# Kernel tuning notes

Measured on AMD Instinct MI355X. Metric: run time of the kernel, lower is better.

Reference implementation:

```python
import jax, jax.numpy as jnp
import numpy as np

B, D, H = 32768, 256, 8
DH = D // H
SCALE = 1.0 / float(np.sqrt(DH))
# neighbor indices: for query node i, context = the other 3 nodes (in order)
NEIGH = np.array([[1, 2, 3], [0, 2, 3], [0, 1, 3], [0, 1, 2]], dtype=np.int32)


def setup_inputs() -> dict:
    key = jax.random.key(0)
    ks = jax.random.split(key, 6)
    s = 0.02
    mk = lambda k: jax.random.normal(k, (D, D), jnp.float32) * s
    return {
        "tokens": jax.random.normal(ks[0], (B, 4, D), jnp.float32),
        "Wq": mk(ks[1]),
        "Wk": mk(ks[2]),
        "Wv": mk(ks[3]),
        "Wr": mk(ks[4]),
        "Wo": mk(ks[5]),
        "ln_g": jnp.ones((D,), jnp.float32),
        "ln_b": jnp.zeros((D,), jnp.float32),
    }


def reference(tokens, Wq, Wk, Wv, Wr, Wo, ln_g, ln_b):
    # tokens: [B,4,D]. All 4 modality queries share one GCA block (share_gca=True),
    # so we batch the 4-node complete-graph message passing into one pass.
    neigh = jnp.asarray(NEIGH)
    ctx = tokens[:, neigh]                    # [B,4,3,D]
    Q = tokens @ Wq.T                         # [B,4,D]
    K = ctx @ Wk.T                            # [B,4,3,D]
    V = ctx @ Wv.T
    R = ctx @ Wr.T
    V_eff = jax.nn.sigmoid(R) * V             # gated values
    Qh = Q.reshape(B, 4, H, DH)
    Kh = K.reshape(B, 4, 3, H, DH)
    Vh = V_eff.reshape(B, 4, 3, H, DH)
    scores = jnp.einsum('bihd,bilhd->bihl', Qh, Kh) * SCALE   # [B,4,H,3]
    attn = jax.nn.softmax(scores, axis=-1)    # dropout = identity (eval mode)
    out = jnp.einsum('bihl,bilhd->bihd', attn, Vh).reshape(B, 4, D)
    out = out @ Wo.T
    y = tokens + out                          # residual
    mu = y.mean(-1, keepdims=True)
    var = y.var(-1, keepdims=True)
    y = (y - mu) / jnp.sqrt(var + 1e-5) * ln_g + ln_b   # LayerNorm
    # attn: [B,4,H,3] -> per-query attn maps (attn[:, i] == attn for modality-i query, [B,H,1,3] squeezed)
    return y, attn
```

## Files before the change

### kernel.cpp

```cpp
#include <hip/hip_runtime.h>
#include <stdint.h>


#define D_DIM   256
#define H_NUM   8
#define RT      64
#define NTHR    512
#define ROWS_TOT 131072
#define Y_SZ    33554432
#define SCALE_F 0.17677669529663687f
#define W_ELEMS 65536
#define WS_NEED (5 * W_ELEMS * 2)

#define SX_LD   264
#define AO_LD   264
#define SP_LD   20

typedef __attribute__((ext_vector_type(8))) short bf16x8;
typedef __attribute__((ext_vector_type(4))) float f32x4;

__device__ __forceinline__ float b2f(uint16_t s) {
    union { uint32_t u; float f; } c; c.u = ((uint32_t)s) << 16; return c.f;
}
__device__ __forceinline__ uint16_t f2b(float f) {
    union { float f; uint32_t u; } c; c.f = f;
    return (uint16_t)((c.u + 0x7fffu + ((c.u >> 16) & 1u)) >> 16);
}
__device__ __forceinline__ bf16x8 cvt8(const float* p) {
    const float4 a = *(const float4*)p;
    const float4 b = *(const float4*)(p + 4);
    bf16x8 r;
    r[0] = (short)f2b(a.x); r[1] = (short)f2b(a.y);
    r[2] = (short)f2b(a.z); r[3] = (short)f2b(a.w);
    r[4] = (short)f2b(b.x); r[5] = (short)f2b(b.y);
    r[6] = (short)f2b(b.z); r[7] = (short)f2b(b.w);
    return r;
}
__device__ __forceinline__ uint2 pack4(f32x4 a) {
    uint2 p;
    p.x = (uint32_t)f2b(a[0]) | ((uint32_t)f2b(a[1]) << 16);
    p.y = (uint32_t)f2b(a[2]) | ((uint32_t)f2b(a[3]) << 16);
    return p;
}

__global__ __launch_bounds__(256)
void conv_weights(const float* __restrict__ Wq, const float* __restrict__ Wk,
                  const float* __restrict__ Wv, const float* __restrict__ Wr,
                  const float* __restrict__ Wo, uint16_t* __restrict__ dst)
{
    const int m = blockIdx.x >> 6;
    const float* src = (m == 0) ? Wq : (m == 1) ? Wk : (m == 2) ? Wv
                     : (m == 3) ? Wr : Wo;
    const int base = (blockIdx.x & 63) * 1024 + threadIdx.x * 4;
    const float4 v = *(const float4*)&src[base];
    uint2 pk;
    pk.x = (uint32_t)f2b(v.x) | ((uint32_t)f2b(v.y) << 16);
    pk.y = (uint32_t)f2b(v.z) | ((uint32_t)f2b(v.w) << 16);
    *(uint2*)&dst[(size_t)m * W_ELEMS + base] = pk;
}

template<bool WBF16>
__global__ __launch_bounds__(NTHR, 2)
void cmaa_fused(const float* __restrict__ tok,
                const float* __restrict__ Wq, const float* __restrict__ Wk,
                const float* __restrict__ Wv, const float* __restrict__ Wr,
                const float* __restrict__ Wo,
                const uint16_t* __restrict__ wbf,
                const float* __restrict__ lng, const float* __restrict__ lnb,
                float* __restrict__ outp)
{
    __shared__ __align__(16) uint16_t sX  [RT * SX_LD];
    __shared__ __align__(16) uint16_t sAO [RT * AO_LD];
    __shared__ __align__(16) float    sALf[RT * H_NUM * 3];
    __shared__ __align__(16) float    sPT [RT * SP_LD];

    const int tid  = threadIdx.x;
    const int wv   = tid >> 6;
    const int lane = tid & 63;
    const int l15  = lane & 15;
    const int quad = lane >> 4;
    const int R0   = blockIdx.x * RT;

    {
        const float* g = tok + (size_t)R0 * D_DIM;
        #pragma unroll
        for (int it = 0; it < 4; ++it) {
            const int t = tid + it * NTHR;
            const int row = t >> 5, c = t & 31;
            *(bf16x8*)&sX[row * SX_LD + c * 8] = cvt8(&g[row * D_DIM + c * 8]);
        }
    }
    __syncthreads();

    const bool qk = (wv < 4);
    const int  hl = wv & 3;

    bf16x8 wo_reg[2][8];

    #pragma unroll
    for (int p = 0; p < 2; ++p) {
        const int h = p * 4 + hl;
        const int colbase = h * 32;
        const float*    WF0 = qk ? Wq : Wv;
        const float*    WF1 = qk ? Wk : Wr;
        const uint16_t* WB0 = wbf + (size_t)(qk ? 0 : 2) * W_ELEMS;
        const uint16_t* WB1 = WB0 + W_ELEMS;

        bf16x8 w0[2][8], w1[2][8];
        #pragma unroll
        for (int ct = 0; ct < 2; ++ct) {
            const int wrow = colbase + ct * 16 + l15;
            #pragma unroll
            for (int kk = 0; kk < 8; ++kk) {
                if constexpr (WBF16) {
                    w0[ct][kk] = *(const bf16x8*)&WB0[(size_t)wrow * D_DIM + kk * 32 + quad * 8];
                    w1[ct][kk] = *(const bf16x8*)&WB1[(size_t)wrow * D_DIM + kk * 32 + quad * 8];
                } else {
                    w0[ct][kk] = cvt8(&WF0[(size_t)wrow * D_DIM + kk * 32 + quad * 8]);
                    w1[ct][kk] = cvt8(&WF1[(size_t)wrow * D_DIM + kk * 32 + quad * 8]);
                }
            }
        }

        f32x4 acc[2][2][4];
        #pragma unroll
        for (int m = 0; m < 2; ++m)
            #pragma unroll
            for (int ct = 0; ct < 2; ++ct)
                #pragma unroll
                for (int nt = 0; nt < 4; ++nt)
                    acc[m][ct][nt] = (f32x4){0.f, 0.f, 0.f, 0.f};

        #pragma unroll
        for (int kk = 0; kk < 8; ++kk) {
            const int k0 = kk * 32;
            bf16x8 ax[4];
            #pragma unroll
            for (int nt = 0; nt < 4; ++nt)
                ax[nt] = *(const bf16x8*)&sX[(nt * 16 + l15) * SX_LD + k0 + quad * 8];
            #pragma unroll
            for (int ct = 0; ct < 2; ++ct)
                #pragma unroll
                for (int nt = 0; nt < 4; ++nt)
                    acc[0][ct][nt] = __builtin_amdgcn_mfma_f32_16x16x32_bf16(w0[ct][kk], ax[nt], acc[0][ct][nt], 0, 0, 0);
            #pragma unroll
            for (int ct = 0; ct < 2; ++ct)
                #pragma unroll
                for (int nt = 0; nt < 4; ++nt)
                    acc[1][ct][nt] = __builtin_amdgcn_mfma_f32_16x16x32_bf16(w1[ct][kk], ax[nt], acc[1][ct][nt], 0, 0, 0);
        }

        if (p == 1) {
            const uint16_t* WoB = wbf + (size_t)4 * W_ELEMS;
            #pragma unroll
            for (int ct = 0; ct < 2; ++ct) {
                const int wrow = wv * 32 + ct * 16 + l15;
                #pragma unroll
                for (int kk = 0; kk < 8; ++kk) {
                    if constexpr (WBF16)
                        wo_reg[ct][kk] = *(const bf16x8*)&WoB[(size_t)wrow * D_DIM + kk * 32 + quad * 8];
                    else
                        wo_reg[ct][kk] = cvt8(&Wo[(size_t)wrow * D_DIM + kk * 32 + quad * 8]);
                }
            }
        }

        if (qk) {
            #pragma unroll
            for (int nt = 0; nt < 4; ++nt) {
                float sc[3];
                #pragma unroll
                for (int m = 1; m <= 3; ++m) {
                    float s = 0.f;
                    #pragma unroll
                    for (int ct = 0; ct < 2; ++ct)
                        #pragma unroll
                        for (int r = 0; r < 4; ++r)
                            s += acc[0][ct][nt][r] * __shfl_xor(acc[1][ct][nt][r], m);
                    s += __shfl_xor(s, 16);
                    s += __shfl_xor(s, 32);
                    sc[m - 1] = s * SCALE_F;
                }
                const float mx = fmaxf(sc[0], fmaxf(sc[1], sc[2]));
                const float e1 = __expf(sc[0] - mx), e2 = __expf(sc[1] - mx), e3 = __expf(sc[2] - mx);
                const float inv = 1.f / (e1 + e2 + e3);
                const float am[3] = { e1 * inv, e2 * inv, e3 * inv };
                const int token = nt * 16 + l15;
                if (quad == 0) {
                    const int ii = token & 3;
                    float* al = &sALf[(token * H_NUM + h) * 3];
                    #pragma unroll
                    for (int l = 0; l < 3; ++l) {
                        const int jj = l + (l >= ii);
                        const int m  = ii ^ jj;
                        al[l] = am[m - 1];
                    }
                }
            }
        } else {
            #pragma unroll
            for (int ct = 0; ct < 2; ++ct)
                #pragma unroll
                for (int nt = 0; nt < 4; ++nt)
                    #pragma unroll
                    for (int r = 0; r < 4; ++r)
                        acc[0][ct][nt][r] *= 1.f / (1.f + __expf(-acc[1][ct][nt][r]));
        }
        __syncthreads();

        if (!qk) {
            #pragma unroll
            for (int nt = 0; nt < 4; ++nt) {
                const int token = nt * 16 + l15;
                const int ii = token & 3;
                const float* al = &sALf[(token * H_NUM + h) * 3];
                float am[3];
                #pragma unroll
                for (int m = 1; m <= 3; ++m) {
                    const int jj = ii ^ m;
                    const int l  = jj - (jj > ii ? 1 : 0);
                    am[m - 1] = al[l];
                }
                #pragma unroll
                for (int ct = 0; ct < 2; ++ct) {
                    f32x4 ao;
                    #pragma unroll
                    for (int r = 0; r < 4; ++r) {
                        const float v = acc[0][ct][nt][r];
                        ao[r] = am[0] * __shfl_xor(v, 1)
                              + am[1] * __shfl_xor(v, 2)
                              + am[2] * __shfl_xor(v, 3);
                    }
                    *(uint2*)&sAO[token * AO_LD + colbase + ct * 16 + quad * 4] = pack4(ao);
                }
            }
        }
        __syncthreads();
    }

    if (tid < 384) {
        const float4 v = *(const float4*)&sALf[tid * 4];
        *(float4*)&outp[Y_SZ + (size_t)R0 * (H_NUM * 3) + tid * 4] = v;
    }

    f32x4 acc3[2][4];
    #pragma unroll
    for (int ct = 0; ct < 2; ++ct)
        #pragma unroll
        for (int nt = 0; nt < 4; ++nt)
            acc3[ct][nt] = (f32x4){0.f, 0.f, 0.f, 0.f};

    #pragma unroll
    for (int kk = 0; kk < 8; ++kk) {
        const int k0 = kk * 32;
        bf16x8 ao[4];
        #pragma unroll
        for (int nt = 0; nt < 4; ++nt)
            ao[nt] = *(const bf16x8*)&sAO[(nt * 16 + l15) * AO_LD + k0 + quad * 8];
        #pragma unroll
        for (int ct = 0; ct < 2; ++ct)
            #pragma unroll
            for (int nt = 0; nt < 4; ++nt)
                acc3[ct][nt] = __builtin_amdgcn_mfma_f32_16x16x32_bf16(wo_reg[ct][kk], ao[nt], acc3[ct][nt], 0, 0, 0);
    }

    #pragma unroll
    for (int nt = 0; nt < 4; ++nt) {
        const int token = nt * 16 + l15;
        float s1 = 0.f, s2 = 0.f;
        #pragma unroll
        for (int ct = 0; ct < 2; ++ct) {
            const ushort4 xv = *(const ushort4*)&sX[token * SX_LD + wv * 32 + ct * 16 + quad * 4];
            const float x0 = b2f(xv.x), x1 = b2f(xv.y), x2 = b2f(xv.z), x3 = b2f(xv.w);
            acc3[ct][nt][0] += x0; acc3[ct][nt][1] += x1;
            acc3[ct][nt][2] += x2; acc3[ct][nt][3] += x3;
            #pragma unroll
            for (int r = 0; r < 4; ++r) {
                const float y = acc3[ct][nt][r];
                s1 += y; s2 += y * y;
            }
        }
        s1 += __shfl_xor(s1, 16); s1 += __shfl_xor(s1, 32);
        s2 += __shfl_xor(s2, 16); s2 += __shfl_xor(s2, 32);
        if (quad == 0) {
            float2 ps; ps.x = s1; ps.y = s2;
            *(float2*)&sPT[token * SP_LD + wv * 2] = ps;
        }
    }
    __syncthreads();

    #pragma unroll
    for (int nt = 0; nt < 4; ++nt) {
        const int token = nt * 16 + l15;
        const f32x4* pp = (const f32x4*)&sPT[token * SP_LD];
        const f32x4 q0 = pp[0], q1 = pp[1], q2 = pp[2], q3 = pp[3];
        const float s1 = q0[0] + q0[2] + q1[0] + q1[2] + q2[0] + q2[2] + q3[0] + q3[2];
        const float s2 = q0[1] + q0[3] + q1[1] + q1[3] + q2[1] + q2[3] + q3[1] + q3[3];
        const float mean = s1 * (1.f / 256.f);
        const float var  = fmaxf(s2 * (1.f / 256.f) - mean * mean, 0.f);
        const float rstd = rsqrtf(var + 1e-5f);
        float* orow = outp + (size_t)(R0 + token) * D_DIM;
        #pragma unroll
        for (int ct = 0; ct < 2; ++ct) {
            const int c0 = wv * 32 + ct * 16 + quad * 4;
            const float4 g4 = *(const float4*)&lng[c0];
            const float4 b4 = *(const float4*)&lnb[c0];
            float4 o4;
            o4.x = (acc3[ct][nt][0] - mean) * rstd * g4.x + b4.x;
            o4.y = (acc3[ct][nt][1] - mean) * rstd * g4.y + b4.y;
            o4.z = (acc3[ct][nt][2] - mean) * rstd * g4.z + b4.z;
            o4.w = (acc3[ct][nt][3] - mean) * rstd * g4.w + b4.w;
            *(float4*)&orow[c0] = o4;
        }
    }
}

extern "C" void kernel_launch(void* const* d_in, const int* in_sizes, int n_in,
                              void* d_out, int out_size, void* d_ws, size_t ws_size,
                              hipStream_t stream) {
    (void)in_sizes; (void)n_in; (void)out_size;
    const float* tok = (const float*)d_in[0];
    const float* Wq  = (const float*)d_in[1];
    const float* Wk  = (const float*)d_in[2];
    const float* Wv  = (const float*)d_in[3];
    const float* Wr  = (const float*)d_in[4];
    const float* Wo  = (const float*)d_in[5];
    const float* lng = (const float*)d_in[6];
    const float* lnb = (const float*)d_in[7];
    float* outp = (float*)d_out;
    uint16_t* wbf = (uint16_t*)d_ws;

    dim3 grid(ROWS_TOT / RT), block(NTHR);
    if (ws_size >= (size_t)WS_NEED) {
        conv_weights<<<dim3(320), dim3(256), 0, stream>>>(Wq, Wk, Wv, Wr, Wo, wbf);
        cmaa_fused<true><<<grid, block, 0, stream>>>(
            tok, Wq, Wk, Wv, Wr, Wo, wbf, lng, lnb, outp);
    } else {
        cmaa_fused<false><<<grid, block, 0, stream>>>(
            tok, Wq, Wk, Wv, Wr, Wo, wbf, lng, lnb, outp);
    }
}
```

Measured before the change: 452.1 us.

## Process two 64-row tiles per block to reuse register-held weights

Each block now handles 128 rows as two 64-row tiles. The Q/K/V/R weight fragments loaded into registers for each head pair are reused across both tiles, and Wo is loaded once after the projection loop. Grid size is halved and the shared-memory buffers are doubled. The intent is to halve global weight reloads per row, at the cost of about double LDS use (likely one block per CU instead of two) and higher register pressure from the two-tile output accumulator.

Result: faster. 414.9 us (-8.2%).

```diff
diff --git a/kernel.cpp b/kernel.cpp
--- a/kernel.cpp
+++ b/kernel.cpp
@@ -69,25 +69,28 @@
                 const float* __restrict__ lng, const float* __restrict__ lnb,
                 float* __restrict__ outp)
 {
-    __shared__ __align__(16) uint16_t sX  [RT * SX_LD];
-    __shared__ __align__(16) uint16_t sAO [RT * AO_LD];
-    __shared__ __align__(16) float    sALf[RT * H_NUM * 3];
-    __shared__ __align__(16) float    sPT [RT * SP_LD];
+    __shared__ __align__(16) uint16_t sX  [2][RT * SX_LD];
+    __shared__ __align__(16) uint16_t sAO [2][RT * AO_LD];
+    __shared__ __align__(16) float    sALf[2][RT * H_NUM * 3];
+    __shared__ __align__(16) float    sPT [2][RT * SP_LD];
 
     const int tid  = threadIdx.x;
     const int wv   = tid >> 6;
     const int lane = tid & 63;
     const int l15  = lane & 15;
     const int quad = lane >> 4;
-    const int R0   = blockIdx.x * RT;
+    const int R0   = blockIdx.x * (2 * RT);
 
     {
         const float* g = tok + (size_t)R0 * D_DIM;
         #pragma unroll
-        for (int it = 0; it < 4; ++it) {
-            const int t = tid + it * NTHR;
-            const int row = t >> 5, c = t & 31;
-            *(bf16x8*)&sX[row * SX_LD + c * 8] = cvt8(&g[row * D_DIM + c * 8]);
+        for (int it = 0; it < 8; ++it) {
+            const int t   = tid + it * NTHR;
+            const int row = t >> 5;
+            const int c   = t & 31;
+            const int tl  = row >> 6;
+            const int rin = row & 63;
+            *(bf16x8*)&sX[tl][rin * SX_LD + c * 8] = cvt8(&g[row * D_DIM + c * 8]);
         }
     }
     __syncthreads();
@@ -95,9 +98,6 @@
     const bool qk = (wv < 4);
     const int  hl = wv & 3;
 
-    bf16x8 wo_reg[2][8];
-
-    #pragma unroll
     for (int p = 0; p < 2; ++p) {
         const int h = p * 4 + hl;
         const int colbase = h * 32;
@@ -123,49 +123,36 @@
         }
 
         f32x4 acc[2][2][4];
-        #pragma unroll
-        for (int m = 0; m < 2; ++m)
-            #pragma unroll
-            for (int ct = 0; ct < 2; ++ct)
+
+        auto gemm = [&](int t) {
+            #pragma unroll
+            for (int m = 0; m < 2; ++m)
+                #pragma unroll
+                for (int ct = 0; ct < 2; ++ct)
+                    #pragma unroll
+                    for (int nt = 0; nt < 4; ++nt)
+                        acc[m][ct][nt] = (f32x4){0.f, 0.f, 0.f, 0.f};
+            #pragma unroll
+            for (int kk = 0; kk < 8; ++kk) {
+                const int k0 = kk * 32;
+                bf16x8 ax[4];
                 #pragma unroll
                 for (int nt = 0; nt < 4; ++nt)
-                    acc[m][ct][nt] = (f32x4){0.f, 0.f, 0.f, 0.f};
-
-        #pragma unroll
-        for (int kk = 0; kk < 8; ++kk) {
-            const int k0 = kk * 32;
-            bf16x8 ax[4];
-            #pragma unroll
-            for (int nt = 0; nt < 4; ++nt)
-                ax[nt] = *(const bf16x8*)&sX[(nt * 16 + l15) * SX_LD + k0 + quad * 8];
-            #pragma unroll
-            for (int ct = 0; ct < 2; ++ct)
-                #pragma unroll
-                for (int nt = 0; nt < 4; ++nt)
-                    acc[0][ct][nt] = __builtin_amdgcn_mfma_f32_16x16x32_bf16(w0[ct][kk], ax[nt], acc[0][ct][nt], 0, 0, 0);
-            #pragma unroll
-            for (int ct = 0; ct < 2; ++ct)
-                #pragma unroll
-                for (int nt = 0; nt < 4; ++nt)
-                    acc[1][ct][nt] = __builtin_amdgcn_mfma_f32_16x16x32_bf16(w1[ct][kk], ax[nt], acc[1][ct][nt], 0, 0, 0);
-        }
-
-        if (p == 1) {
-            const uint16_t* WoB = wbf + (size_t)4 * W_ELEMS;
-            #pragma unroll
-            for (int ct = 0; ct < 2; ++ct) {
-                const int wrow = wv * 32 + ct * 16 + l15;
-                #pragma unroll
-                for (int kk = 0; kk < 8; ++kk) {
-                    if constexpr (WBF16)
-                        wo_reg[ct][kk] = *(const bf16x8*)&WoB[(size_t)wrow * D_DIM + kk * 32 + quad * 8];
-                    else
-                        wo_reg[ct][kk] = cvt8(&Wo[(size_t)wrow * D_DIM + kk * 32 + quad * 8]);
-                }
-            }
-        }
-
-        if (qk) {
+                    ax[nt] = *(const bf16x8*)&sX[t][(nt * 16 + l15) * SX_LD + k0 + quad * 8];
+                #pragma unroll
+                for (int ct = 0; ct < 2; ++ct)
+                    #pragma unroll
+                    for (int nt = 0; nt < 4; ++nt)
+                        acc[0][ct][nt] = __builtin_amdgcn_mfma_f32_16x16x32_bf16(w0[ct][kk], ax[nt], acc[0][ct][nt], 0, 0, 0);
+                #pragma unroll
+                for (int ct = 0; ct < 2; ++ct)
+                    #pragma unroll
+                    for (int nt = 0; nt < 4; ++nt)
+                        acc[1][ct][nt] = __builtin_amdgcn_mfma_f32_16x16x32_bf16(w1[ct][kk], ax[nt], acc[1][ct][nt], 0, 0, 0);
+            }
+        };
+
+        auto qk_post = [&](int t) {
             #pragma unroll
             for (int nt = 0; nt < 4; ++nt) {
                 float sc[3];
@@ -188,7 +175,7 @@
                 const int token = nt * 16 + l15;
                 if (quad == 0) {
                     const int ii = token & 3;
-                    float* al = &sALf[(token * H_NUM + h) * 3];
+                    float* al = &sALf[t][(token * H_NUM + h) * 3];
                     #pragma unroll
                     for (int l = 0; l < 3; ++l) {
                         const int jj = l + (l >= ii);
@@ -197,7 +184,9 @@
                     }
                 }
             }
-        } else {
+        };
+
+        auto v_post = [&]() {
             #pragma unroll
             for (int ct = 0; ct < 2; ++ct)
                 #pragma unroll
@@ -205,15 +194,14 @@
                     #pragma unroll
                     for (int r = 0; r < 4; ++r)
                         acc[0][ct][nt][r] *= 1.f / (1.f + __expf(-acc[1][ct][nt][r]));
-        }
-        __syncthreads();
-
-        if (!qk) {
+        };
+
+        auto pv = [&](int t) {
             #pragma unroll
             for (int nt = 0; nt < 4; ++nt) {
                 const int token = nt * 16 + l15;
                 const int ii = token & 3;
-                const float* al = &sALf[(token * H_NUM + h) * 3];
+                const float* al = &sALf[t][(token * H_NUM + h) * 3];
                 float am[3];
                 #pragma unroll
                 for (int m = 1; m <= 3; ++m) {
@@ -231,86 +219,121 @@
                               + am[1] * __shfl_xor(v, 2)
                               + am[2] * __shfl_xor(v, 3);
                     }
-                    *(uint2*)&sAO[token * AO_LD + colbase + ct * 16 + quad * 4] = pack4(ao);
-                }
-            }
-        }
+                    *(uint2*)&sAO[t][token * AO_LD + colbase + ct * 16 + quad * 4] = pack4(ao);
+                }
+            }
+        };
+
+        gemm(0);
+        if (qk) qk_post(0); else v_post();
         __syncthreads();
-    }
-
-    if (tid < 384) {
-        const float4 v = *(const float4*)&sALf[tid * 4];
-        *(float4*)&outp[Y_SZ + (size_t)R0 * (H_NUM * 3) + tid * 4] = v;
-    }
-
-    f32x4 acc3[2][4];
+        if (!qk) pv(0);
+        gemm(1);
+        if (qk) qk_post(1); else v_post();
+        __syncthreads();
+        if (!qk) pv(1);
+    }
+
+    bf16x8 wo_reg[2][8];
+    {
+        const uint16_t* WoB = wbf + (size_t)4 * W_ELEMS;
+        #pragma unroll
+        for (int ct = 0; ct < 2; ++ct) {
+            const int wrow = wv * 32 + ct * 16 + l15;
+            #pragma unroll
+            for (int kk = 0; kk < 8; ++kk) {
+                if constexpr (WBF16)
+                    wo_reg[ct][kk] = *(const bf16x8*)&WoB[(size_t)wrow * D_DIM + kk * 32 + quad * 8];
+                else
+                    wo_reg[ct][kk] = cvt8(&Wo[(size_t)wrow * D_DIM + kk * 32 + quad * 8]);
+            }
+        }
+    }
+    __syncthreads();
+
+    {
+        const float* sa = &sALf[0][0];
+        #pragma unroll
+        for (int i = tid; i < 768; i += NTHR) {
+            const float4 v = *(const float4*)&sa[i * 4];
+            *(float4*)&outp[Y_SZ + (size_t)R0 * 24 + (size_t)i * 4] = v;
+        }
+    }
+
+    f32x4 acc3[2][2][4];
     #pragma unroll
-    for (int ct = 0; ct < 2; ++ct)
-        #pragma unroll
-        for (int nt = 0; nt < 4; ++nt)
-            acc3[ct][nt] = (f32x4){0.f, 0.f, 0.f, 0.f};
+    for (int t = 0; t < 2; ++t) {
+        #pragma unroll
+        for (int ct = 0; ct < 2; ++ct)
+            #pragma unroll
+            for (int nt = 0; nt < 4; ++nt)
+                acc3[t][ct][nt] = (f32x4){0.f, 0.f, 0.f, 0.f};
+
+        #pragma unroll
+        for (int kk = 0; kk < 8; ++kk) {
+            const int k0 = kk * 32;
+            bf16x8 ao[4];
+            #pragma unroll
+            for (int nt = 0; nt < 4; ++nt)
+                ao[nt] = *(const bf16x8*)&sAO[t][(nt * 16 + l15) * AO_LD + k0 + quad * 8];
+            #pragma unroll
+            for (int ct = 0; ct < 2; ++ct)
+                #pragma unroll
+                for (int nt = 0; nt < 4; ++nt)
+                    acc3[t][ct][nt] = __builtin_amdgcn_mfma_f32_16x16x32_bf16(wo_reg[ct][kk], ao[nt], acc3[t][ct][nt], 0, 0, 0);
+        }
+
+        #pragma unroll
+        for (int nt = 0; nt < 4; ++nt) {
+            const int token = nt * 16 + l15;
+            float s1 = 0.f, s2 = 0.f;
+            #pragma unroll
+            for (int ct = 0; ct < 2; ++ct) {
+                const ushort4 xv = *(const ushort4*)&sX[t][token * SX_LD + wv * 32 + ct * 16 + quad * 4];
+                const float x0 = b2f(xv.x), x1 = b2f(xv.y), x2 = b2f(xv.z), x3 = b2f(xv.w);
+                acc3[t][ct][nt][0] += x0; acc3[t][ct][nt][1] += x1;
+                acc3[t][ct][nt][2] += x2; acc3[t][ct][nt][3] += x3;
+                #pragma unroll
+                for (int r = 0; r < 4; ++r) {
+                    const float y = acc3[t][ct][nt][r];
+                    s1 += y; s2 += y * y;
+                }
+            }
+            s1 += __shfl_xor(s1, 16); s1 += __shfl_xor(s1, 32);
+            s2 += __shfl_xor(s2, 16); s2 += __shfl_xor(s2, 32);
+            if (quad == 0) {
+                float2 ps; ps.x = s1; ps.y = s2;
+                *(float2*)&sPT[t][token * SP_LD + wv * 2] = ps;
+            }
+        }
+    }
+    __syncthreads();
 
     #pragma unroll
-    for (int kk = 0; kk < 8; ++kk) {
-        const int k0 = kk * 32;
-        bf16x8 ao[4];
-        #pragma unroll
-        for (int nt = 0; nt < 4; ++nt)
-            ao[nt] = *(const bf16x8*)&sAO[(nt * 16 + l15) * AO_LD + k0 + quad * 8];
-        #pragma unroll
-        for (int ct = 0; ct < 2; ++ct)
-            #pragma unroll
-            for (int nt = 0; nt < 4; ++nt)
-                acc3[ct][nt] = __builtin_amdgcn_mfma_f32_16x16x32_bf16(wo_reg[ct][kk], ao[nt], acc3[ct][nt], 0, 0, 0);
-    }
-
-    #pragma unroll
-    for (int nt = 0; nt < 4; ++nt) {
-        const int token = nt * 16 + l15;
-        float s1 = 0.f, s2 = 0.f;
-        #pragma unroll
-        for (int ct = 0; ct < 2; ++ct) {
-            const ushort4 xv = *(const ushort4*)&sX[token * SX_LD + wv * 32 + ct * 16 + quad * 4];
-            const float x0 = b2f(xv.x), x1 = b2f(xv.y), x2 = b2f(xv.z), x3 = b2f(xv.w);
-            acc3[ct][nt][0] += x0; acc3[ct][nt][1] += x1;
-            acc3[ct][nt][2] += x2; acc3[ct][nt][3] += x3;
-            #pragma unroll
-            for (int r = 0; r < 4; ++r) {
-                const float y = acc3[ct][nt][r];
-                s1 += y; s2 += y * y;
-            }
-        }
-        s1 += __shfl_xor(s1, 16); s1 += __shfl_xor(s1, 32);
-        s2 += __shfl_xor(s2, 16); s2 += __shfl_xor(s2, 32);
-        if (quad == 0) {
-            float2 ps; ps.x = s1; ps.y = s2;
-            *(float2*)&sPT[token * SP_LD + wv * 2] = ps;
-        }
-    }
-    __syncthreads();
-
-    #pragma unroll
-    for (int nt = 0; nt < 4; ++nt) {
-        const int token = nt * 16 + l15;
-        const f32x4* pp = (const f32x4*)&sPT[token * SP_LD];
-        const f32x4 q0 = pp[0], q1 = pp[1], q2 = pp[2], q3 = pp[3];
-        const float s1 = q0[0] + q0[2] + q1[0] + q1[2] + q2[0] + q2[2] + q3[0] + q3[2];
-        const float s2 = q0[1] + q0[3] + q1[1] + q1[3] + q2[1] + q2[3] + q3[1] + q3[3];
-        const float mean = s1 * (1.f / 256.f);
-        const float var  = fmaxf(s2 * (1.f / 256.f) - mean * mean, 0.f);
-        const float rstd = rsqrtf(var + 1e-5f);
-        float* orow = outp + (size_t)(R0 + token) * D_DIM;
-        #pragma unroll
-        for (int ct = 0; ct < 2; ++ct) {
-            const int c0 = wv * 32 + ct * 16 + quad * 4;
-            const float4 g4 = *(const float4*)&lng[c0];
-            const float4 b4 = *(const float4*)&lnb[c0];
-            float4 o4;
-            o4.x = (acc3[ct][nt][0] - mean) * rstd * g4.x + b4.x;
-            o4.y = (acc3[ct][nt][1] - mean) * rstd * g4.y + b4.y;
-            o4.z = (acc3[ct][nt][2] - mean) * rstd * g4.z + b4.z;
-            o4.w = (acc3[ct][nt][3] - mean) * rstd * g4.w + b4.w;
-            *(float4*)&orow[c0] = o4;
+    for (int t = 0; t < 2; ++t) {
+        #pragma unroll
+        for (int nt = 0; nt < 4; ++nt) {
+            const int token = nt * 16 + l15;
+            const f32x4* pp = (const f32x4*)&sPT[t][token * SP_LD];
+            const f32x4 q0 = pp[0], q1 = pp[1], q2 = pp[2], q3 = pp[3];
+            const float s1 = q0[0] + q0[2] + q1[0] + q1[2] + q2[0] + q2[2] + q3[0] + q3[2];
+            const float s2 = q0[1] + q0[3] + q1[1] + q1[3] + q2[1] + q2[3] + q3[1] + q3[3];
+            const float mean = s1 * (1.f / 256.f);
+            const float var  = fmaxf(s2 * (1.f / 256.f) - mean * mean, 0.f);
+            const float rstd = rsqrtf(var + 1e-5f);
+            float* orow = outp + (size_t)(R0 + t * RT + token) * D_DIM;
+            #pragma unroll
+            for (int ct = 0; ct < 2; ++ct) {
+                const int c0 = wv * 32 + ct * 16 + quad * 4;
+                const float4 g4 = *(const float4*)&lng[c0];
+                const float4 b4 = *(const float4*)&lnb[c0];
+                float4 o4;
+                o4.x = (acc3[t][ct][nt][0] - mean) * rstd * g4.x + b4.x;
+                o4.y = (acc3[t][ct][nt][1] - mean) * rstd * g4.y + b4.y;
+                o4.z = (acc3[t][ct][nt][2] - mean) * rstd * g4.z + b4.z;
+                o4.w = (acc3[t][ct][nt][3] - mean) * rstd * g4.w + b4.w;
+                *(float4*)&orow[c0] = o4;
+            }
         }
     }
 }
@@ -330,7 +353,7 @@
     float* outp = (float*)d_out;
     uint16_t* wbf = (uint16_t*)d_ws;
 
-    dim3 grid(ROWS_TOT / RT), block(NTHR);
+    dim3 grid(ROWS_TOT / (2 * RT)), block(NTHR);
     if (ws_size >= (size_t)WS_NEED) {
         conv_weights<<<dim3(320), dim3(256), 0, stream>>>(Wq, Wk, Wv, Wr, Wo, wbf);
         cmaa_fused<true><<<grid, block, 0, stream>>>(
```
